# Performance work log

Measured on AMD Instinct MI355X. Metric: run time of the kernel, lower is better.

The kernel has to match this reference:

```python
import jax, jax.numpy as jnp
import numpy as np

H = 512          # hidden_size
L = 1024         # total sequence length (q_len + c_len + t_len)
C = 512          # number of columns (key/value length)
NUM_REL = 51     # len(relations2id)


def setup_inputs() -> dict:
    key = jax.random.key(0)
    ks = jax.random.split(key, 12)
    w = 1.0 / np.sqrt(H)  # torch nn.Linear default init scale
    return {
        "query": jax.random.normal(ks[0], (1, L, H), jnp.float32),
        "key": jax.random.normal(ks[1], (1, C, H), jnp.float32),
        "value": jax.random.normal(ks[2], (1, C, H), jnp.float32),
        "predefined_relation": jax.random.randint(ks[3], (L, L), 0, NUM_REL, dtype=jnp.int32),
        "q_len": 384,
        "c_len": 512,
        "Wq": jax.random.uniform(ks[4], (H, H), jnp.float32, -w, w),
        "bq": jnp.zeros((H,), jnp.float32),
        "Wk": jax.random.uniform(ks[5], (H, H), jnp.float32, -w, w),
        "bk": jnp.zeros((H,), jnp.float32),
        "Wv": jax.random.uniform(ks[6], (H, H), jnp.float32, -w, w),
        "bv": jnp.zeros((H,), jnp.float32),
        "rel_k_emb": jax.random.normal(ks[7], (NUM_REL, H), jnp.float32),
        "rel_v_emb": jax.random.normal(ks[8], (NUM_REL, H), jnp.float32),
    }


def reference(query, key, value, predefined_relation, q_len, c_len,
              Wq, bq, Wk, bk, Wv, bv, rel_k_emb, rel_v_emb):
    # --- get_fixed_column_relation (kind='column', enable_latent_relations=False) ---
    # predefined_relation: [L, L] relation ids; take column block [L, C]
    mc = predefined_relation[:, q_len:q_len + c_len]          # [L, C]
    relation_k = rel_k_emb[mc]                                # [L, C, H]
    relation_v = rel_v_emb[mc]                                # [L, C, H] (value path discarded by forward)
    # --- single-head projections (nbatches == 1) ---
    q = query[0] @ Wq.T + bq                                  # [L, H]
    k = key[0] @ Wk.T + bk                                    # [C, H]
    v = value[0] @ Wv.T + bv                                  # [C, H]
    # --- relative_attention_logits ---
    qk = q @ k.T                                              # [L, C]
    q_rel = jnp.einsum('lh,lch->lc', q, relation_k)           # per-query relation scores [L, C]
    scores = (qk + q_rel) / np.sqrt(H).astype(np.float32)
    attn = jax.nn.softmax(scores, axis=-1)                    # [L, C]
    # forward returns self.attn[0, 0] (the pre-dropout attention probabilities);
    # relative_attention_values output (attn @ v + einsum('lc,lch->lh', attn, relation_v))
    # is computed in the torch module but discarded, so we return only attn.
    return attn
```

## Files before the change

kernel.cpp:

```cpp
#include <hip/hip_runtime.h>
#include <hip/hip_bf16.h>

#define HH 512
#define LL 1024
#define CC 512
#define NREL 51

typedef __attribute__((ext_vector_type(8))) short bf16x8;
typedef __attribute__((ext_vector_type(4))) float f32x4;

__device__ __forceinline__ short f2bn(float f) {
    return __builtin_bit_cast(short, __float2bfloat16(f));
}

__device__ __forceinline__ void gl16(const void* g, void* l) {
    __builtin_amdgcn_global_load_lds(
        (const __attribute__((address_space(1))) void*)g,
        (__attribute__((address_space(3))) void*)l, 16, 0, 0);
}

__global__ __launch_bounds__(256) void k0_prep(
    const float* __restrict__ query, const float* __restrict__ key,
    const float* __restrict__ Wq, const float* __restrict__ Wk,
    const float* __restrict__ relk,
    short* __restrict__ queryb, short* __restrict__ keyb,
    short* __restrict__ Wqb, short* __restrict__ Wkb, short* __restrict__ relkb)
{
    for (int u = blockIdx.x * 256 + threadIdx.x; u < 167104; u += 131072) {
        const float* src; short* dst; int c;
        if (u < 65536)       { src = query; dst = queryb; c = u; }
        else if (u < 98304)  { src = key;   dst = keyb;   c = u - 65536; }
        else if (u < 131072) { src = Wq;    dst = Wqb;    c = u - 98304; }
        else if (u < 163840) { src = Wk;    dst = Wkb;    c = u - 131072; }
        else                 { src = relk;  dst = relkb;  c = u - 163840; }
        float4 x = *(const float4*)(src + c * 8);
        float4 y = *(const float4*)(src + c * 8 + 4);
        bf16x8 o;
        o[0] = f2bn(x.x); o[1] = f2bn(x.y); o[2] = f2bn(x.z); o[3] = f2bn(x.w);
        o[4] = f2bn(y.x); o[5] = f2bn(y.y); o[6] = f2bn(y.z); o[7] = f2bn(y.w);
        const int cs = c ^ ((c >> 6) & 7);
        *(bf16x8*)(dst + cs * 8) = o;
    }
}

__global__ __launch_bounds__(64) void k1_proj(
    const short* __restrict__ queryb, const short* __restrict__ keyb,
    const short* __restrict__ Wqb, const short* __restrict__ Wkb,
    const float* __restrict__ bq,
    short* __restrict__ qbuf, short* __restrict__ kbuf)
{
    __shared__ __align__(16) short buf[2][5120];
    const int b = blockIdx.x, l = threadIdx.x;
    const short *A, *B; const float* bias; short* outp; int m0, n0;
    if (b < 512) { A = queryb; B = Wqb; bias = bq;      outp = qbuf;
                   m0 = (b >> 3) * 16; n0 = (b & 7) * 64; }
    else         { const int bb = b - 512; A = keyb; B = Wkb; bias = nullptr; outp = kbuf;
                   m0 = (bb >> 3) * 16; n0 = (bb & 7) * 64; }
    const int lr = l & 15, lk = (l >> 4) * 8;
    const int lx = 8 * (lr & 7);
    const int srow = l >> 3, scol = (l & 7) * 8;

#define K1_STAGE(bi, t) do { \
        const int k0 = (t) * 64; \
        short* Lb = buf[bi]; \
        _Pragma("unroll") \
        for (int j = 0; j < 2; ++j) \
            gl16(A + (m0 + j * 8 + srow) * HH + k0 + scol, Lb + j * 512); \
        _Pragma("unroll") \
        for (int j = 0; j < 8; ++j) \
            gl16(B + (n0 + j * 8 + srow) * HH + k0 + scol, Lb + 1024 + j * 512); \
    } while (0)

    f32x4 acc[4] = {};
#define K1_COMP(bi) do { \
        const short* Lb = buf[bi]; \
        bf16x8 a0 = *(const bf16x8*)(Lb + lr * 64 + ((0 + lk) ^ lx)); \
        bf16x8 a1 = *(const bf16x8*)(Lb + lr * 64 + ((32 + lk) ^ lx)); \
        _Pragma("unroll") \
        for (int f = 0; f < 4; ++f) { \
            bf16x8 b0 = *(const bf16x8*)(Lb + 1024 + (f * 16 + lr) * 64 + ((0 + lk) ^ lx)); \
            bf16x8 b1 = *(const bf16x8*)(Lb + 1024 + (f * 16 + lr) * 64 + ((32 + lk) ^ lx)); \
            acc[f] = __builtin_amdgcn_mfma_f32_16x16x32_bf16(a0, b0, acc[f], 0, 0, 0); \
            acc[f] = __builtin_amdgcn_mfma_f32_16x16x32_bf16(a1, b1, acc[f], 0, 0, 0); \
        } \
    } while (0)

    K1_STAGE(0, 0);
    #pragma unroll
    for (int t = 0; t < 8; ++t) {
        if (t < 7) {
            K1_STAGE((t + 1) & 1, t + 1);
            asm volatile("s_waitcnt vmcnt(10)" ::: "memory");
        } else {
            asm volatile("s_waitcnt vmcnt(0)" ::: "memory");
        }
        __builtin_amdgcn_sched_barrier(0);
        K1_COMP(t & 1);
    }
#undef K1_STAGE
#undef K1_COMP

    #pragma unroll
    for (int f = 0; f < 4; ++f) {
        const int colg = f * 16 + lr;
        const float bv = bias ? bias[n0 + colg] : 0.f;
        #pragma unroll
        for (int r = 0; r < 4; ++r) {
            const int row = m0 + (l >> 4) * 4 + r;
            outp[row * HH + n0 + (colg ^ (8 * (row & 7)))] = f2bn(acc[f][r] + bv);
        }
    }
}

__global__ __launch_bounds__(64) void k2_attn(
    const short* __restrict__ qbuf, const short* __restrict__ kbuf,
    const short* __restrict__ relkb, const int* __restrict__ rel,
    const int* __restrict__ qlen, float* __restrict__ Ssum,
    float* __restrict__ out)
{
    __shared__ __align__(16) short buf[3][9216];
    __shared__ float Rs[16][64];
    const int b = blockIdx.x, l = threadIdx.x;
    const int l0 = (b >> 3) * 16, cg = b & 7, cb = cg * 64;
    const int lr = l & 15, lk = (l >> 4) * 8;
    const int lx = 8 * (lr & 7);
    const int srow = l >> 3, scol = (l & 7) * 8;
    const int qoff = qlen[0];

    int idxr[4][4];
    #pragma unroll
    for (int r = 0; r < 4; ++r) {
        const int row = (l >> 4) * 4 + r;
        #pragma unroll
        for (int f = 0; f < 4; ++f)
            idxr[r][f] = rel[(l0 + row) * LL + qoff + cb + f * 16 + lr];
    }

#define K2_STAGE(bi, t) do { \
        const int k0 = (t) * 64; \
        short* Lb = buf[bi]; \
        _Pragma("unroll") \
        for (int j = 0; j < 2; ++j) \
            gl16(qbuf + (l0 + j * 8 + srow) * HH + k0 + scol, Lb + j * 512); \
        _Pragma("unroll") \
        for (int j = 0; j < 8; ++j) \
            gl16(kbuf + (cb + j * 8 + srow) * HH + k0 + scol, Lb + 1024 + j * 512); \
        _Pragma("unroll") \
        for (int j = 0; j < 8; ++j) \
            gl16(relkb + (j * 8 + srow) * HH + k0 + scol, Lb + 5120 + j * 512); \
    } while (0)

    f32x4 acc[4] = {}, racc[4] = {};
#define K2_COMP(bi) do { \
        const short* Lb = buf[bi]; \
        bf16x8 a0 = *(const bf16x8*)(Lb + lr * 64 + ((0 + lk) ^ lx)); \
        bf16x8 a1 = *(const bf16x8*)(Lb + lr * 64 + ((32 + lk) ^ lx)); \
        _Pragma("unroll") \
        for (int f = 0; f < 4; ++f) { \
            const int ro = (f * 16 + lr) * 64; \
            bf16x8 k0v = *(const bf16x8*)(Lb + 1024 + ro + ((0 + lk) ^ lx)); \
            bf16x8 k1v = *(const bf16x8*)(Lb + 1024 + ro + ((32 + lk) ^ lx)); \
            bf16x8 r0v = *(const bf16x8*)(Lb + 5120 + ro + ((0 + lk) ^ lx)); \
            bf16x8 r1v = *(const bf16x8*)(Lb + 5120 + ro + ((32 + lk) ^ lx)); \
            acc[f]  = __builtin_amdgcn_mfma_f32_16x16x32_bf16(a0, k0v, acc[f], 0, 0, 0); \
            acc[f]  = __builtin_amdgcn_mfma_f32_16x16x32_bf16(a1, k1v, acc[f], 0, 0, 0); \
            racc[f] = __builtin_amdgcn_mfma_f32_16x16x32_bf16(a0, r0v, racc[f], 0, 0, 0); \
            racc[f] = __builtin_amdgcn_mfma_f32_16x16x32_bf16(a1, r1v, racc[f], 0, 0, 0); \
        } \
    } while (0)

    K2_STAGE(0, 0); K2_STAGE(1, 1);
    #pragma unroll
    for (int t = 0; t < 8; ++t) {
        if (t < 6) {
            K2_STAGE((t + 2) % 3, t + 2);
            asm volatile("s_waitcnt vmcnt(36)" ::: "memory");
        } else if (t == 6) {
            asm volatile("s_waitcnt vmcnt(18)" ::: "memory");
        } else {
            asm volatile("s_waitcnt vmcnt(0)" ::: "memory");
        }
        __builtin_amdgcn_sched_barrier(0);
        K2_COMP(t % 3);
    }
#undef K2_STAGE
#undef K2_COMP

    #pragma unroll
    for (int f = 0; f < 4; ++f)
        #pragma unroll
        for (int r = 0; r < 4; ++r)
            Rs[(l >> 4) * 4 + r][f * 16 + lr] = racc[f][r];
    __syncthreads();

    const float scale = 0.04419417382415922f;
    #pragma unroll
    for (int r = 0; r < 4; ++r) {
        const int row = (l >> 4) * 4 + r;
        float s = 0.f;
        #pragma unroll
        for (int f = 0; f < 4; ++f) {
            float e = __expf((acc[f][r] + Rs[row][idxr[r][f]]) * scale);
            acc[f][r] = e; s += e;
        }
        #pragma unroll
        for (int sh = 1; sh < 16; sh <<= 1) s += __shfl_xor(s, sh, 64);
        if (lr == 0) Ssum[(l0 + row) * 8 + cg] = s;
    }
    #pragma unroll
    for (int f = 0; f < 4; ++f)
        #pragma unroll
        for (int r = 0; r < 4; ++r) {
            const int row = (l >> 4) * 4 + r;
            out[(l0 + row) * CC + cb + f * 16 + lr] = acc[f][r];
        }
}

__global__ __launch_bounds__(256) void k3_norm(
    const float* __restrict__ Ssum, float* __restrict__ out)
{
    const int e = (blockIdx.x * 256 + threadIdx.x) * 4;
    const int row = e >> 9;
    float4 s0 = *(const float4*)(Ssum + row * 8);
    float4 s1 = *(const float4*)(Ssum + row * 8 + 4);
    const float inv = 1.f / (s0.x + s0.y + s0.z + s0.w + s1.x + s1.y + s1.z + s1.w);
    float4 v = *(float4*)(out + e);
    v.x *= inv; v.y *= inv; v.z *= inv; v.w *= inv;
    *(float4*)(out + e) = v;
}

extern "C" void kernel_launch(void* const* d_in, const int* in_sizes, int n_in,
                              void* d_out, int out_size, void* d_ws, size_t ws_size,
                              hipStream_t stream) {
    const float* query = (const float*)d_in[0];
    const float* key   = (const float*)d_in[1];
    const int*   rel   = (const int*)d_in[3];
    const int*   qlen  = (const int*)d_in[4];
    const float* Wq    = (const float*)d_in[6];
    const float* bq    = (const float*)d_in[7];
    const float* Wk    = (const float*)d_in[8];
    const float* relk  = (const float*)d_in[12];

    float* out = (float*)d_out;
    short* p = (short*)d_ws;
    short* queryb = p;  p += LL * HH;
    short* keyb   = p;  p += CC * HH;
    short* Wqb    = p;  p += HH * HH;
    short* Wkb    = p;  p += HH * HH;
    short* relkb  = p;  p += 64 * HH;
    short* qbuf   = p;  p += LL * HH;
    short* kbuf   = p;  p += CC * HH;
    float* Ssum   = (float*)p;

    k0_prep<<<512, 256, 0, stream>>>(query, key, Wq, Wk, relk,
                                     queryb, keyb, Wqb, Wkb, relkb);
    k1_proj<<<768, 64, 0, stream>>>(queryb, keyb, Wqb, Wkb, bq, qbuf, kbuf);
    k2_attn<<<512, 64, 0, stream>>>(qbuf, kbuf, relkb, rel, qlen, Ssum, out);
    k3_norm<<<512, 256, 0, stream>>>(Ssum, out);
}
```

Baseline: 25.74 us.

## Move relation-score GEMM into projection epilogue and fuse normalization via last-block counter

Computes the q·rel_k relation scores in the q-projection epilogue: each block takes its freshly produced 16x64 q tile and runs it against the matching rel_k columns, accumulating into a global [L,64] buffer with atomics. The attention kernel then drops the relation MFMAs and their LDS staging, and just gathers the relation scores. The separate normalization kernel is removed; the last of the 8 column blocks per row group, found through an atomic counter, rescales the output rows. Zeroing of the atomic buffers and counters is added to the prep kernel. The risks are float atomic ordering nondeterminism and a serialized tail pass by the last block in each row group.

```diff
diff --git a/kernel.cpp b/kernel.cpp
--- a/kernel.cpp
+++ b/kernel.cpp
@@ -24,8 +24,13 @@
     const float* __restrict__ Wq, const float* __restrict__ Wk,
     const float* __restrict__ relk,
     short* __restrict__ queryb, short* __restrict__ keyb,
-    short* __restrict__ Wqb, short* __restrict__ Wkb, short* __restrict__ relkb)
+    short* __restrict__ Wqb, short* __restrict__ Wkb, short* __restrict__ relkb,
+    float* __restrict__ zbase)
 {
+    const int z = blockIdx.x * 256 + threadIdx.x;
+    const float4 zz = make_float4(0.f, 0.f, 0.f, 0.f);
+    if (z < 16400) ((float4*)zbase)[z] = zz;
+    if (z < 832)  ((float4*)(relkb + 51 * HH))[z] = zz;
     for (int u = blockIdx.x * 256 + threadIdx.x; u < 167104; u += 131072) {
         const float* src; short* dst; int c;
         if (u < 65536)       { src = query; dst = queryb; c = u; }
@@ -46,19 +51,28 @@
 __global__ __launch_bounds__(64) void k1_proj(
     const short* __restrict__ queryb, const short* __restrict__ keyb,
     const short* __restrict__ Wqb, const short* __restrict__ Wkb,
-    const float* __restrict__ bq,
-    short* __restrict__ qbuf, short* __restrict__ kbuf)
+    const short* __restrict__ relkb, const float* __restrict__ bq,
+    short* __restrict__ qbuf, short* __restrict__ kbuf,
+    float* __restrict__ Rbuf)
 {
     __shared__ __align__(16) short buf[2][5120];
+    __shared__ __align__(16) short rl[5120];
     const int b = blockIdx.x, l = threadIdx.x;
-    const short *A, *B; const float* bias; short* outp; int m0, n0;
-    if (b < 512) { A = queryb; B = Wqb; bias = bq;      outp = qbuf;
-                   m0 = (b >> 3) * 16; n0 = (b & 7) * 64; }
-    else         { const int bb = b - 512; A = keyb; B = Wkb; bias = nullptr; outp = kbuf;
-                   m0 = (bb >> 3) * 16; n0 = (bb & 7) * 64; }
+    const bool isq = (b < 512);
+    const short *A, *B; short* outp; int m0, n0;
+    if (isq) { A = queryb; B = Wqb; outp = qbuf;
+               m0 = (b >> 3) * 16; n0 = (b & 7) * 64; }
+    else     { const int bb = b - 512; A = keyb; B = Wkb; outp = kbuf;
+               m0 = (bb >> 3) * 16; n0 = (bb & 7) * 64; }
     const int lr = l & 15, lk = (l >> 4) * 8;
     const int lx = 8 * (lr & 7);
     const int srow = l >> 3, scol = (l & 7) * 8;
+
+    if (isq) {
+        #pragma unroll
+        for (int j = 0; j < 8; ++j)
+            gl16(relkb + (j * 8 + srow) * HH + n0 + scol, rl + j * 512);
+    }
 
 #define K1_STAGE(bi, t) do { \
         const int k0 = (t) * 64; \
@@ -100,26 +114,56 @@
 #undef K1_STAGE
 #undef K1_COMP
 
-    #pragma unroll
-    for (int f = 0; f < 4; ++f) {
-        const int colg = f * 16 + lr;
-        const float bv = bias ? bias[n0 + colg] : 0.f;
-        #pragma unroll
-        for (int r = 0; r < 4; ++r) {
-            const int row = m0 + (l >> 4) * 4 + r;
-            outp[row * HH + n0 + (colg ^ (8 * (row & 7)))] = f2bn(acc[f][r] + bv);
+    if (isq) {
+        short* qt = rl + 4096;
+        #pragma unroll
+        for (int f = 0; f < 4; ++f) {
+            const int colg = f * 16 + lr;
+            const float bv = bq[n0 + colg];
+            #pragma unroll
+            for (int r = 0; r < 4; ++r) {
+                const int row = (l >> 4) * 4 + r;
+                const short h = f2bn(acc[f][r] + bv);
+                outp[(m0 + row) * HH + n0 + (colg ^ (8 * (row & 7)))] = h;
+                qt[row * 64 + (((colg >> 3) ^ (row & 7)) << 3) + (colg & 7)] = h;
+            }
+        }
+        f32x4 racc[4] = {};
+        bf16x8 a0 = *(const bf16x8*)(qt + lr * 64 + ((0 + lk) ^ lx));
+        bf16x8 a1 = *(const bf16x8*)(qt + lr * 64 + ((32 + lk) ^ lx));
+        #pragma unroll
+        for (int f = 0; f < 4; ++f) {
+            bf16x8 b0 = *(const bf16x8*)(rl + (f * 16 + lr) * 64 + ((0 + lk) ^ lx));
+            bf16x8 b1 = *(const bf16x8*)(rl + (f * 16 + lr) * 64 + ((32 + lk) ^ lx));
+            racc[f] = __builtin_amdgcn_mfma_f32_16x16x32_bf16(a0, b0, racc[f], 0, 0, 0);
+            racc[f] = __builtin_amdgcn_mfma_f32_16x16x32_bf16(a1, b1, racc[f], 0, 0, 0);
+        }
+        #pragma unroll
+        for (int f = 0; f < 4; ++f)
+            #pragma unroll
+            for (int r = 0; r < 4; ++r)
+                atomicAdd(Rbuf + (m0 + (l >> 4) * 4 + r) * 64 + f * 16 + lr,
+                          racc[f][r]);
+    } else {
+        #pragma unroll
+        for (int f = 0; f < 4; ++f) {
+            const int colg = f * 16 + lr;
+            #pragma unroll
+            for (int r = 0; r < 4; ++r) {
+                const int row = m0 + (l >> 4) * 4 + r;
+                outp[row * HH + n0 + (colg ^ (8 * (row & 7)))] = f2bn(acc[f][r]);
+            }
         }
     }
 }
 
 __global__ __launch_bounds__(64) void k2_attn(
     const short* __restrict__ qbuf, const short* __restrict__ kbuf,
-    const short* __restrict__ relkb, const int* __restrict__ rel,
-    const int* __restrict__ qlen, float* __restrict__ Ssum,
-    float* __restrict__ out)
+    const int* __restrict__ rel, const int* __restrict__ qlen,
+    const float* __restrict__ Rbuf, float* __restrict__ Ssum,
+    int* __restrict__ cnt, float* __restrict__ out)
 {
-    __shared__ __align__(16) short buf[3][9216];
-    __shared__ float Rs[16][64];
+    __shared__ __align__(16) short buf[3][5120];
     const int b = blockIdx.x, l = threadIdx.x;
     const int l0 = (b >> 3) * 16, cg = b & 7, cb = cg * 64;
     const int lr = l & 15, lk = (l >> 4) * 8;
@@ -145,12 +189,9 @@
         _Pragma("unroll") \
         for (int j = 0; j < 8; ++j) \
             gl16(kbuf + (cb + j * 8 + srow) * HH + k0 + scol, Lb + 1024 + j * 512); \
-        _Pragma("unroll") \
-        for (int j = 0; j < 8; ++j) \
-            gl16(relkb + (j * 8 + srow) * HH + k0 + scol, Lb + 5120 + j * 512); \
     } while (0)
 
-    f32x4 acc[4] = {}, racc[4] = {};
+    f32x4 acc[4] = {};
 #define K2_COMP(bi) do { \
         const short* Lb = buf[bi]; \
         bf16x8 a0 = *(const bf16x8*)(Lb + lr * 64 + ((0 + lk) ^ lx)); \
@@ -160,23 +201,25 @@
             const int ro = (f * 16 + lr) * 64; \
             bf16x8 k0v = *(const bf16x8*)(Lb + 1024 + ro + ((0 + lk) ^ lx)); \
             bf16x8 k1v = *(const bf16x8*)(Lb + 1024 + ro + ((32 + lk) ^ lx)); \
-            bf16x8 r0v = *(const bf16x8*)(Lb + 5120 + ro + ((0 + lk) ^ lx)); \
-            bf16x8 r1v = *(const bf16x8*)(Lb + 5120 + ro + ((32 + lk) ^ lx)); \
-            acc[f]  = __builtin_amdgcn_mfma_f32_16x16x32_bf16(a0, k0v, acc[f], 0, 0, 0); \
-            acc[f]  = __builtin_amdgcn_mfma_f32_16x16x32_bf16(a1, k1v, acc[f], 0, 0, 0); \
-            racc[f] = __builtin_amdgcn_mfma_f32_16x16x32_bf16(a0, r0v, racc[f], 0, 0, 0); \
-            racc[f] = __builtin_amdgcn_mfma_f32_16x16x32_bf16(a1, r1v, racc[f], 0, 0, 0); \
+            acc[f] = __builtin_amdgcn_mfma_f32_16x16x32_bf16(a0, k0v, acc[f], 0, 0, 0); \
+            acc[f] = __builtin_amdgcn_mfma_f32_16x16x32_bf16(a1, k1v, acc[f], 0, 0, 0); \
         } \
     } while (0)
 
+    float rv[4][4];
     K2_STAGE(0, 0); K2_STAGE(1, 1);
     #pragma unroll
     for (int t = 0; t < 8; ++t) {
         if (t < 6) {
             K2_STAGE((t + 2) % 3, t + 2);
-            asm volatile("s_waitcnt vmcnt(36)" ::: "memory");
+            asm volatile("s_waitcnt vmcnt(20)" ::: "memory");
         } else if (t == 6) {
-            asm volatile("s_waitcnt vmcnt(18)" ::: "memory");
+            asm volatile("s_waitcnt vmcnt(10)" ::: "memory");
+            #pragma unroll
+            for (int r = 0; r < 4; ++r)
+                #pragma unroll
+                for (int f = 0; f < 4; ++f)
+                    rv[r][f] = Rbuf[(l0 + (l >> 4) * 4 + r) * 64 + idxr[r][f]];
         } else {
             asm volatile("s_waitcnt vmcnt(0)" ::: "memory");
         }
@@ -185,13 +228,6 @@
     }
 #undef K2_STAGE
 #undef K2_COMP
-
-    #pragma unroll
-    for (int f = 0; f < 4; ++f)
-        #pragma unroll
-        for (int r = 0; r < 4; ++r)
-            Rs[(l >> 4) * 4 + r][f * 16 + lr] = racc[f][r];
-    __syncthreads();
 
     const float scale = 0.04419417382415922f;
     #pragma unroll
@@ -200,7 +236,7 @@
         float s = 0.f;
         #pragma unroll
         for (int f = 0; f < 4; ++f) {
-            float e = __expf((acc[f][r] + Rs[row][idxr[r][f]]) * scale);
+            float e = __expf((acc[f][r] + rv[r][f]) * scale);
             acc[f][r] = e; s += e;
         }
         #pragma unroll
@@ -214,19 +250,31 @@
             const int row = (l >> 4) * 4 + r;
             out[(l0 + row) * CC + cb + f * 16 + lr] = acc[f][r];
         }
-}
-
-__global__ __launch_bounds__(256) void k3_norm(
-    const float* __restrict__ Ssum, float* __restrict__ out)
-{
-    const int e = (blockIdx.x * 256 + threadIdx.x) * 4;
-    const int row = e >> 9;
-    float4 s0 = *(const float4*)(Ssum + row * 8);
-    float4 s1 = *(const float4*)(Ssum + row * 8 + 4);
-    const float inv = 1.f / (s0.x + s0.y + s0.z + s0.w + s1.x + s1.y + s1.z + s1.w);
-    float4 v = *(float4*)(out + e);
-    v.x *= inv; v.y *= inv; v.z *= inv; v.w *= inv;
-    *(float4*)(out + e) = v;
+
+    __threadfence();
+    int old = 0;
+    if (l == 0)
+        old = __hip_atomic_fetch_add(&cnt[b >> 3], 1, __ATOMIC_ACQ_REL,
+                                     __HIP_MEMORY_SCOPE_AGENT);
+    old = __shfl(old, 0, 64);
+    if (old == 7) {
+        __threadfence();
+        float inv = 1.f;
+        if (l < 16) {
+            const float* sp = Ssum + (l0 + l) * 8;
+            inv = 1.f / (sp[0] + sp[1] + sp[2] + sp[3] +
+                         sp[4] + sp[5] + sp[6] + sp[7]);
+        }
+        #pragma unroll
+        for (int row = 0; row < 16; ++row) {
+            const float iv = __shfl(inv, row, 64);
+            float4* po = (float4*)(out + (l0 + row) * CC);
+            float4 v0 = po[l], v1 = po[l + 64];
+            v0.x *= iv; v0.y *= iv; v0.z *= iv; v0.w *= iv;
+            v1.x *= iv; v1.y *= iv; v1.z *= iv; v1.w *= iv;
+            po[l] = v0; po[l + 64] = v1;
+        }
+    }
 }
 
 extern "C" void kernel_launch(void* const* d_in, const int* in_sizes, int n_in,
@@ -251,10 +299,12 @@
     short* qbuf   = p;  p += LL * HH;
     short* kbuf   = p;  p += CC * HH;
     float* Ssum   = (float*)p;
+    float* Rbuf   = Ssum + LL * 8;
+    int*   cnt    = (int*)(Rbuf + LL * 64);
 
     k0_prep<<<512, 256, 0, stream>>>(query, key, Wq, Wk, relk,
-                                     queryb, keyb, Wqb, Wkb, relkb);
-    k1_proj<<<768, 64, 0, stream>>>(queryb, keyb, Wqb, Wkb, bq, qbuf, kbuf);
-    k2_attn<<<512, 64, 0, stream>>>(qbuf, kbuf, relkb, rel, qlen, Ssum, out);
-    k3_norm<<<512, 256, 0, stream>>>(Ssum, out);
-}
+                                     queryb, keyb, Wqb, Wkb, relkb, Rbuf);
+    k1_proj<<<768, 64, 0, stream>>>(queryb, keyb, Wqb, Wkb, relkb, bq,
+                                    qbuf, kbuf, Rbuf);
+    k2_attn<<<512, 64, 0, stream>>>(qbuf, kbuf, rel, qlen, Rbuf, Ssum, cnt, out);
+}
```

After: 55.72 us. +116.4%, slower.
